# Kernel tuning notes

Measured on AMD Instinct MI355X. Metric: run time of the kernel, lower is better.

The kernel has to match this reference:

```python
import jax, jax.numpy as jnp
import numpy as np

GROUP_SIZE = 64

def _dequant(wq, scale, zero):
    # HQQ groupwise dequant: W = (Wq - zero) * scale, groups along input dim.
    out_dim, in_dim = wq.shape
    g = in_dim // GROUP_SIZE
    w = (wq.astype(jnp.float32).reshape(out_dim, g, GROUP_SIZE) - zero[:, :, None]) * scale[:, :, None]
    return w.reshape(out_dim, in_dim)

def setup_inputs() -> dict:
    key = jax.random.key(0)
    ks = jax.random.split(key, 10)
    T, H, I = 256, 4096, 14336
    G1, G2 = H // GROUP_SIZE, I // GROUP_SIZE  # 64, 224
    x = jax.random.normal(ks[0], (T, H), dtype=jnp.float32)
    w1_q = jax.random.randint(ks[1], (I, H), 0, 16, dtype=jnp.int32)
    w1_scale = jax.random.uniform(ks[2], (I, G1), dtype=jnp.float32) * 0.02
    w1_zero = jax.random.uniform(ks[3], (I, G1), dtype=jnp.float32) * 8.0
    w3_q = jax.random.randint(ks[4], (I, H), 0, 16, dtype=jnp.int32)
    w3_scale = jax.random.uniform(ks[5], (I, G1), dtype=jnp.float32) * 0.02
    w3_zero = jax.random.uniform(ks[6], (I, G1), dtype=jnp.float32) * 8.0
    w2_q = jax.random.randint(ks[7], (H, I), 0, 16, dtype=jnp.int32)
    w2_scale = jax.random.uniform(ks[8], (H, G2), dtype=jnp.float32) * 0.02
    w2_zero = jax.random.uniform(ks[9], (H, G2), dtype=jnp.float32) * 8.0
    return {"x": x, "w1_q": w1_q, "w1_scale": w1_scale, "w1_zero": w1_zero,
            "w3_q": w3_q, "w3_scale": w3_scale, "w3_zero": w3_zero,
            "w2_q": w2_q, "w2_scale": w2_scale, "w2_zero": w2_zero}

def reference(x, w1_q, w1_scale, w1_zero, w3_q, w3_scale, w3_zero, w2_q, w2_scale, w2_zero):
    w1 = _dequant(w1_q, w1_scale, w1_zero)  # [I, H]
    w3 = _dequant(w3_q, w3_scale, w3_zero)  # [I, H]
    w2 = _dequant(w2_q, w2_scale, w2_zero)  # [H, I]
    gate = jax.nn.silu(jnp.einsum('th,ih->ti', x, w1))  # [T, I]
    up = jnp.einsum('th,ih->ti', x, w3)                 # [T, I]
    return jnp.einsum('ti,hi->th', gate * up, w2)       # [T, H]
```

## Files before the change

### kernel.cpp

```cpp
#include <hip/hip_runtime.h>
#include <cstdint>
#include <cstddef>

#define T_DIM 256
#define H_DIM 4096
#define I_DIM 14336

typedef __attribute__((ext_vector_type(8))) short s8v;
typedef __attribute__((ext_vector_type(4))) short s4v;
typedef __attribute__((ext_vector_type(4))) float f4v;

static constexpr size_t XS_BYTES   = (size_t)T_DIM * H_DIM * 2;
static constexpr size_t ACT_OFF    = XS_BYTES;
static constexpr size_t ACT_BYTES  = (size_t)T_DIM * I_DIM * 2;
static constexpr size_t PART_OFF   = ACT_OFF + ACT_BYTES;
static constexpr size_t PART_BYTES = 4ull * T_DIM * H_DIM * 4;
static constexpr size_t WS_NEEDED  = PART_OFF + PART_BYTES;

__device__ __forceinline__ unsigned short f2bf(float f) {
    unsigned u = __builtin_bit_cast(unsigned, f);
    u += 0x7fffu + ((u >> 16) & 1u);
    return (unsigned short)(u >> 16);
}

__device__ __forceinline__ void bar_read() {
    __builtin_amdgcn_sched_barrier(0);
    __builtin_amdgcn_s_barrier();
    __builtin_amdgcn_sched_barrier(0);
}
__device__ __forceinline__ void bar_write() {
    __builtin_amdgcn_sched_barrier(0);
    asm volatile("s_waitcnt lgkmcnt(0)" ::: "memory");
    __builtin_amdgcn_s_barrier();
    __builtin_amdgcn_sched_barrier(0);
}

__device__ __forceinline__ s4v dq4(const int4 q, float s, float ns) {
    union { unsigned short u[4]; s4v v; } r;
    r.u[0] = f2bf(fmaf((float)q.x, s, ns));
    r.u[1] = f2bf(fmaf((float)q.y, s, ns));
    r.u[2] = f2bf(fmaf((float)q.z, s, ns));
    r.u[3] = f2bf(fmaf((float)q.w, s, ns));
    return r.v;
}

__global__ __launch_bounds__(256) void k_prep(const float* __restrict__ x,
                                              unsigned short* __restrict__ xs) {
    int i = (blockIdx.x * 256 + threadIdx.x) * 8;
    float4 a = *(const float4*)(x + i);
    float4 b = *(const float4*)(x + i + 4);
    union { unsigned short u[8]; s8v v; } r;
    r.u[0] = f2bf(a.x); r.u[1] = f2bf(a.y); r.u[2] = f2bf(a.z); r.u[3] = f2bf(a.w);
    r.u[4] = f2bf(b.x); r.u[5] = f2bf(b.y); r.u[6] = f2bf(b.z); r.u[7] = f2bf(b.w);
    *(s8v*)(xs + i) = r.v;
}

struct S1 { int4 q1, q3; float s1, z1, s3, z3; };

__global__ __launch_bounds__(512, 4) void k_gemm1(
    const int* __restrict__ w1q, const float* __restrict__ w1s, const float* __restrict__ w1z,
    const int* __restrict__ w3q, const float* __restrict__ w3s, const float* __restrict__ w3z,
    const unsigned short* __restrict__ xs, unsigned short* __restrict__ act)
{
    __shared__ unsigned char lds[2][8192];
    const int tid  = threadIdx.x;
    const int swz  = (blockIdx.x & 7) * 56 + (blockIdx.x >> 3);
    const int n0   = swz * 32;
    const int wid  = tid >> 6;
    const int lane = tid & 63;
    const int lr   = lane & 15;
    const int lkb  = lane >> 4;

    const int row = tid >> 4, h = tid & 15;
    const int4* w1p = (const int4*)w1q + (size_t)(n0 + row) * 1024;
    const int4* w3p = (const int4*)w3q + (size_t)(n0 + row) * 1024;
    const float* s1p = w1s + (size_t)(n0 + row) * 64;
    const float* z1p = w1z + (size_t)(n0 + row) * 64;
    const float* s3p = w3s + (size_t)(n0 + row) * 64;
    const float* z3p = w3z + (size_t)(n0 + row) * 64;
    const int wbyte = row * 128 + (((h >> 1) ^ (row & 7)) << 4) + ((h & 1) << 3);

    const unsigned char* xsb = (const unsigned char*)xs;

    f4v accg[2][2], accu[2][2];
    const f4v fz = {0.f, 0.f, 0.f, 0.f};
    #pragma unroll
    for (int i = 0; i < 2; ++i)
        #pragma unroll
        for (int j = 0; j < 2; ++j) { accg[i][j] = fz; accu[i][j] = fz; }

    auto load = [&](int kt, S1& p) {
        p.q1 = w1p[kt * 16 + h];
        p.q3 = w3p[kt * 16 + h];
        p.s1 = s1p[kt]; p.z1 = z1p[kt];
        p.s3 = s3p[kt]; p.z3 = z3p[kt];
    };
    auto store = [&](const S1& p, unsigned char* b) {
        *(s4v*)(b + wbyte)        = dq4(p.q1, p.s1, -p.z1 * p.s1);
        *(s4v*)(b + 4096 + wbyte) = dq4(p.q3, p.s3, -p.z3 * p.s3);
    };
    auto compute = [&](const unsigned char* b, int kt) {
        #pragma unroll
        for (int kf = 0; kf < 2; ++kf) {
            const int sw = kf * 4 + lkb;
            s8v a[2], b1[2], b3[2];
            #pragma unroll
            for (int nf = 0; nf < 2; ++nf) {
                const int rbo = (nf * 16 + lr) * 128 + ((sw ^ (lr & 7)) << 4);
                b1[nf] = *(const s8v*)(b + rbo);
                b3[nf] = *(const s8v*)(b + 4096 + rbo);
            }
            #pragma unroll
            for (int mf = 0; mf < 2; ++mf)
                a[mf] = *(const s8v*)(xsb + (size_t)(wid * 32 + mf * 16 + lr) * 8192
                                          + kt * 128 + kf * 64 + lkb * 16);
            #pragma unroll
            for (int mf = 0; mf < 2; ++mf)
                #pragma unroll
                for (int nf = 0; nf < 2; ++nf) {
                    accg[mf][nf] = __builtin_amdgcn_mfma_f32_16x16x32_bf16(a[mf], b1[nf], accg[mf][nf], 0, 0, 0);
                    accu[mf][nf] = __builtin_amdgcn_mfma_f32_16x16x32_bf16(a[mf], b3[nf], accu[mf][nf], 0, 0, 0);
                }
        }
    };

    S1 A, B;
    load(0, A);
    store(A, lds[0]);
    load(1, B);
    bar_write();

    for (int it = 0; it < 32; ++it) {
        const int t = it * 2;
        load(t + 2 > 63 ? 63 : t + 2, A);
        compute(lds[0], t);
        bar_read();
        store(B, lds[1]);
        bar_write();
        load(t + 3 > 63 ? 63 : t + 3, B);
        compute(lds[1], t + 1);
        bar_read();
        store(A, lds[0]);
        bar_write();
    }

    unsigned char* actb = (unsigned char*)act;
    #pragma unroll
    for (int mf = 0; mf < 2; ++mf)
        #pragma unroll
        for (int nf = 0; nf < 2; ++nf)
            #pragma unroll
            for (int r = 0; r < 4; ++r) {
                const int m = wid * 32 + mf * 16 + lkb * 4 + r;
                const int n = n0 + nf * 16 + lr;
                float g = accg[mf][nf][r];
                float u = accu[mf][nf][r];
                float sg = g / (1.0f + __expf(-g));
                *(unsigned short*)(actb + (size_t)m * (I_DIM * 2) + n * 2) = f2bf(sg * u);
            }
}

struct S2 { int4 q2; float s2, z2; };

template<bool ATOMIC>
__global__ __launch_bounds__(512, 4) void k_gemm2(
    const int* __restrict__ w2q, const float* __restrict__ w2s, const float* __restrict__ w2z,
    const unsigned short* __restrict__ act, float* __restrict__ outp)
{
    __shared__ unsigned char lds[2][4096];
    const int tid  = threadIdx.x;
    const int swz  = (blockIdx.x & 7) * 64 + (blockIdx.x >> 3);
    const int kc   = swz >> 7;
    const int nb   = swz & 127;
    const int n0   = nb * 32;
    const int wid  = tid >> 6;
    const int lane = tid & 63;
    const int lr   = lane & 15;
    const int lkb  = lane >> 4;

    const int row = tid >> 4, h = tid & 15;
    const int4* w2p = (const int4*)w2q + (size_t)(n0 + row) * 3584 + (size_t)kc * 896;
    const float* s2p = w2s + (size_t)(n0 + row) * 224 + kc * 56;
    const float* z2p = w2z + (size_t)(n0 + row) * 224 + kc * 56;
    const int wbyte = row * 128 + (((h >> 1) ^ (row & 7)) << 4) + ((h & 1) << 3);

    const unsigned char* actb = (const unsigned char*)act;
    const size_t akc = (size_t)kc * 7168;

    f4v acc[2][2];
    const f4v fz = {0.f, 0.f, 0.f, 0.f};
    #pragma unroll
    for (int i = 0; i < 2; ++i) { acc[i][0] = fz; acc[i][1] = fz; }

    auto load = [&](int kt, S2& p) {
        p.q2 = w2p[kt * 16 + h];
        p.s2 = s2p[kt]; p.z2 = z2p[kt];
    };
    auto store = [&](const S2& p, unsigned char* b) {
        *(s4v*)(b + wbyte) = dq4(p.q2, p.s2, -p.z2 * p.s2);
    };
    auto compute = [&](const unsigned char* b, int kt) {
        #pragma unroll
        for (int kf = 0; kf < 2; ++kf) {
            const int sw = kf * 4 + lkb;
            s8v a[2], b2[2];
            #pragma unroll
            for (int nf = 0; nf < 2; ++nf)
                b2[nf] = *(const s8v*)(b + (nf * 16 + lr) * 128 + ((sw ^ (lr & 7)) << 4));
            #pragma unroll
            for (int mf = 0; mf < 2; ++mf)
                a[mf] = *(const s8v*)(actb + (size_t)(wid * 32 + mf * 16 + lr) * (I_DIM * 2)
                                          + akc + kt * 128 + kf * 64 + lkb * 16);
            #pragma unroll
            for (int mf = 0; mf < 2; ++mf)
                #pragma unroll
                for (int nf = 0; nf < 2; ++nf)
                    acc[mf][nf] = __builtin_amdgcn_mfma_f32_16x16x32_bf16(a[mf], b2[nf], acc[mf][nf], 0, 0, 0);
        }
    };

    S2 A, B;
    load(0, A);
    store(A, lds[0]);
    load(1, B);
    bar_write();

    for (int it = 0; it < 28; ++it) {
        const int t = it * 2;
        load(t + 2 > 55 ? 55 : t + 2, A);
        compute(lds[0], t);
        bar_read();
        store(B, lds[1]);
        bar_write();
        load(t + 3 > 55 ? 55 : t + 3, B);
        compute(lds[1], t + 1);
        bar_read();
        store(A, lds[0]);
        bar_write();
    }

    float* pout = outp + (ATOMIC ? 0 : (size_t)kc * ((size_t)T_DIM * H_DIM));
    #pragma unroll
    for (int mf = 0; mf < 2; ++mf)
        #pragma unroll
        for (int nf = 0; nf < 2; ++nf)
            #pragma unroll
            for (int r = 0; r < 4; ++r) {
                const int m = wid * 32 + mf * 16 + lkb * 4 + r;
                const int n = n0 + nf * 16 + lr;
                if (ATOMIC) atomicAdd(&outp[(size_t)m * H_DIM + n], acc[mf][nf][r]);
                else        pout[(size_t)m * H_DIM + n] = acc[mf][nf][r];
            }
}

__global__ __launch_bounds__(256) void k_reduce(const f4v* __restrict__ p,
                                                f4v* __restrict__ o) {
    int i = blockIdx.x * 256 + threadIdx.x;
    f4v s = p[i];
    #pragma unroll
    for (int c = 1; c < 4; ++c) s += p[(size_t)c * 262144 + i];
    o[i] = s;
}

__global__ __launch_bounds__(256) void k_zero(f4v* __restrict__ o) {
    o[blockIdx.x * 256 + threadIdx.x] = (f4v){0.f, 0.f, 0.f, 0.f};
}

extern "C" void kernel_launch(void* const* d_in, const int* in_sizes, int n_in,
                              void* d_out, int out_size, void* d_ws, size_t ws_size,
                              hipStream_t stream) {
    const float* x   = (const float*)d_in[0];
    const int*   w1q = (const int*)  d_in[1];
    const float* w1s = (const float*)d_in[2];
    const float* w1z = (const float*)d_in[3];
    const int*   w3q = (const int*)  d_in[4];
    const float* w3s = (const float*)d_in[5];
    const float* w3z = (const float*)d_in[6];
    const int*   w2q = (const int*)  d_in[7];
    const float* w2s = (const float*)d_in[8];
    const float* w2z = (const float*)d_in[9];
    float* outp = (float*)d_out;

    unsigned short* xs  = (unsigned short*)d_ws;
    unsigned short* act = (unsigned short*)((char*)d_ws + ACT_OFF);
    float*          prt = (float*)((char*)d_ws + PART_OFF);
    const bool partials = (ws_size >= WS_NEEDED);

    k_prep<<<512, 256, 0, stream>>>(x, xs);
    k_gemm1<<<448, 512, 0, stream>>>(w1q, w1s, w1z, w3q, w3s, w3z, xs, act);
    if (partials) {
        k_gemm2<false><<<512, 512, 0, stream>>>(w2q, w2s, w2z, act, prt);
        k_reduce<<<1024, 256, 0, stream>>>((const f4v*)prt, (f4v*)outp);
    } else {
        k_zero<<<1024, 256, 0, stream>>>((f4v*)outp);
        k_gemm2<true><<<512, 512, 0, stream>>>(w2q, w2s, w2z, act, outp);
    }
}
```

Before: 334.9 us.

## Stage activations into LDS via async global_load_lds with deeper pipelining

Activations (bf16 x and the intermediate act) are re-laid out in MFMA fragment order so each block can copy whole k-tiles into a 4-deep LDS ring with direct global-to-LDS loads, instead of each wave reading A fragments straight from global memory. Weight register prefetch is deepened to four stages, with explicit vmcnt waits, and block swizzles are changed. The LDS footprint grows to roughly 140KB per block, which drops occupancy to one block per CU, and the hand-tuned vmcnt counts must match the exact number of issued loads.

```diff
diff --git a/kernel.cpp b/kernel.cpp
--- a/kernel.cpp
+++ b/kernel.cpp
@@ -21,6 +21,13 @@
     unsigned u = __builtin_bit_cast(unsigned, f);
     u += 0x7fffu + ((u >> 16) & 1u);
     return (unsigned short)(u >> 16);
+}
+
+__device__ __forceinline__ void g2lds16(const void* g, void* l) {
+    __builtin_amdgcn_global_load_lds(
+        (const __attribute__((address_space(1))) unsigned int*)g,
+        (__attribute__((address_space(3))) unsigned int*)l,
+        16, 0, 0);
 }
 
 __device__ __forceinline__ void bar_read() {
@@ -46,26 +53,31 @@
 
 __global__ __launch_bounds__(256) void k_prep(const float* __restrict__ x,
                                               unsigned short* __restrict__ xs) {
-    int i = (blockIdx.x * 256 + threadIdx.x) * 8;
-    float4 a = *(const float4*)(x + i);
-    float4 b = *(const float4*)(x + i + 4);
+    int t = blockIdx.x * 256 + threadIdx.x;
+    int l = t & 63, f = t >> 6;
+    int msub = f & 15, ksub = f >> 4;
+    int m = msub * 16 + (l & 15);
+    int k = ksub * 32 + (l >> 4) * 8;
+    const float* xp = x + (size_t)m * H_DIM + k;
+    float4 a = *(const float4*)xp;
+    float4 b = *(const float4*)(xp + 4);
     union { unsigned short u[8]; s8v v; } r;
     r.u[0] = f2bf(a.x); r.u[1] = f2bf(a.y); r.u[2] = f2bf(a.z); r.u[3] = f2bf(a.w);
     r.u[4] = f2bf(b.x); r.u[5] = f2bf(b.y); r.u[6] = f2bf(b.z); r.u[7] = f2bf(b.w);
-    *(s8v*)(xs + i) = r.v;
-}
-
-struct S1 { int4 q1, q3; float s1, z1, s3, z3; };
-
-__global__ __launch_bounds__(512, 4) void k_gemm1(
+    *((s8v*)xs + t) = r.v;
+}
+
+struct W1R { int4 q1, q3; float s1, z1, s3, z3; };
+
+__global__ __launch_bounds__(512) void k_gemm1(
     const int* __restrict__ w1q, const float* __restrict__ w1s, const float* __restrict__ w1z,
     const int* __restrict__ w3q, const float* __restrict__ w3s, const float* __restrict__ w3z,
     const unsigned short* __restrict__ xs, unsigned short* __restrict__ act)
 {
-    __shared__ unsigned char lds[2][8192];
+    __shared__ unsigned char lds[147456];
     const int tid  = threadIdx.x;
-    const int swz  = (blockIdx.x & 7) * 56 + (blockIdx.x >> 3);
-    const int n0   = swz * 32;
+    const int blk  = blockIdx.x;
+    const int n0   = blk * 32;
     const int wid  = tid >> 6;
     const int lane = tid & 63;
     const int lr   = lane & 15;
@@ -78,7 +90,7 @@
     const float* z1p = w1z + (size_t)(n0 + row) * 64;
     const float* s3p = w3s + (size_t)(n0 + row) * 64;
     const float* z3p = w3z + (size_t)(n0 + row) * 64;
-    const int wbyte = row * 128 + (((h >> 1) ^ (row & 7)) << 4) + ((h & 1) << 3);
+    const int wbyte = row * 128 + ((((h >> 1) ^ (row & 7)) << 4) | ((h & 1) << 3));
 
     const unsigned char* xsb = (const unsigned char*)xs;
 
@@ -89,31 +101,38 @@
         #pragma unroll
         for (int j = 0; j < 2; ++j) { accg[i][j] = fz; accu[i][j] = fz; }
 
-    auto load = [&](int kt, S1& p) {
+    auto xl = [&](int t) -> unsigned char* { return lds + (size_t)(t & 3) * 32768; };
+    auto wl = [&](int t) -> unsigned char* { return lds + 131072 + (size_t)(t & 1) * 8192; };
+
+    auto wload = [&](int kt, W1R& p) {
         p.q1 = w1p[kt * 16 + h];
         p.q3 = w3p[kt * 16 + h];
-        p.s1 = s1p[kt]; p.z1 = z1p[kt];
-        p.s3 = s3p[kt]; p.z3 = z3p[kt];
-    };
-    auto store = [&](const S1& p, unsigned char* b) {
+        p.s1 = s1p[kt]; p.z1 = z1p[kt]; p.s3 = s3p[kt]; p.z3 = z3p[kt];
+    };
+    auto xstage = [&](int kt, unsigned char* dst) {
+        const unsigned char* src = xsb + (size_t)kt * 32768 + (size_t)(wid * 4) * 1024
+                                       + (size_t)lane * 16;
+        #pragma unroll
+        for (int j = 0; j < 4; ++j)
+            g2lds16(src + j * 1024, dst + (wid * 4 + j) * 1024);
+    };
+    auto wstore = [&](const W1R& p, unsigned char* b) {
         *(s4v*)(b + wbyte)        = dq4(p.q1, p.s1, -p.z1 * p.s1);
         *(s4v*)(b + 4096 + wbyte) = dq4(p.q3, p.s3, -p.z3 * p.s3);
     };
-    auto compute = [&](const unsigned char* b, int kt) {
+    auto compute = [&](const unsigned char* xb, const unsigned char* wb) {
         #pragma unroll
         for (int kf = 0; kf < 2; ++kf) {
-            const int sw = kf * 4 + lkb;
             s8v a[2], b1[2], b3[2];
             #pragma unroll
+            for (int mf = 0; mf < 2; ++mf)
+                a[mf] = *(const s8v*)(xb + (kf * 16 + wid * 2 + mf) * 1024 + lane * 16);
+            #pragma unroll
             for (int nf = 0; nf < 2; ++nf) {
-                const int rbo = (nf * 16 + lr) * 128 + ((sw ^ (lr & 7)) << 4);
-                b1[nf] = *(const s8v*)(b + rbo);
-                b3[nf] = *(const s8v*)(b + 4096 + rbo);
+                const int rbo = (nf * 16 + lr) * 128 + (((kf * 4 + lkb) ^ (lr & 7)) << 4);
+                b1[nf] = *(const s8v*)(wb + rbo);
+                b3[nf] = *(const s8v*)(wb + 4096 + rbo);
             }
-            #pragma unroll
-            for (int mf = 0; mf < 2; ++mf)
-                a[mf] = *(const s8v*)(xsb + (size_t)(wid * 32 + mf * 16 + lr) * 8192
-                                          + kt * 128 + kf * 64 + lkb * 16);
             #pragma unroll
             for (int mf = 0; mf < 2; ++mf)
                 #pragma unroll
@@ -124,54 +143,66 @@
         }
     };
 
-    S1 A, B;
-    load(0, A);
-    store(A, lds[0]);
-    load(1, B);
+    W1R R0, R1, R2, R3;
+    wload(0, R0);
+    wload(1, R1); xstage(0, xl(0));
+    wload(2, R2); xstage(1, xl(1));
+    wload(3, R3); xstage(2, xl(2));
+    wstore(R0, wl(0));
     bar_write();
 
-    for (int it = 0; it < 32; ++it) {
-        const int t = it * 2;
-        load(t + 2 > 63 ? 63 : t + 2, A);
-        compute(lds[0], t);
+    auto step = [&](int t, W1R& Rld, const W1R& Rst) {
+        wload((t + 4) & 63, Rld);
+        __builtin_amdgcn_sched_barrier(0);
+        xstage((t + 3) & 63, xl(t + 3));
+        __builtin_amdgcn_sched_barrier(0);
+        asm volatile("s_waitcnt vmcnt(26)" ::: "memory");
+        __builtin_amdgcn_sched_barrier(0);
+        compute(xl(t), wl(t));
         bar_read();
-        store(B, lds[1]);
+        wstore(Rst, wl(t + 1));
         bar_write();
-        load(t + 3 > 63 ? 63 : t + 3, B);
-        compute(lds[1], t + 1);
-        bar_read();
-        store(A, lds[0]);
-        bar_write();
+    };
+    for (int i = 0; i < 16; ++i) {
+        const int t = i * 4;
+        step(t + 0, R0, R1);
+        step(t + 1, R1, R2);
+        step(t + 2, R2, R3);
+        step(t + 3, R3, R0);
     }
 
     unsigned char* actb = (unsigned char*)act;
     #pragma unroll
-    for (int mf = 0; mf < 2; ++mf)
+    for (int mf = 0; mf < 2; ++mf) {
+        const int msub = wid * 2 + mf;
         #pragma unroll
         for (int nf = 0; nf < 2; ++nf)
             #pragma unroll
             for (int r = 0; r < 4; ++r) {
-                const int m = wid * 32 + mf * 16 + lkb * 4 + r;
-                const int n = n0 + nf * 16 + lr;
+                const int mrow  = lkb * 4 + r;
+                const int n     = nf * 16 + lr;
+                const int lanef = mrow + (n >> 3) * 16;
                 float g = accg[mf][nf][r];
                 float u = accu[mf][nf][r];
                 float sg = g / (1.0f + __expf(-g));
-                *(unsigned short*)(actb + (size_t)m * (I_DIM * 2) + n * 2) = f2bf(sg * u);
+                *(unsigned short*)(actb + (size_t)(blk * 16 + msub) * 1024
+                                        + lanef * 16 + (n & 7) * 2) = f2bf(sg * u);
             }
-}
-
-struct S2 { int4 q2; float s2, z2; };
+    }
+}
+
+struct W2R { int4 q2; float s2, z2; };
 
 template<bool ATOMIC>
-__global__ __launch_bounds__(512, 4) void k_gemm2(
+__global__ __launch_bounds__(512) void k_gemm2(
     const int* __restrict__ w2q, const float* __restrict__ w2s, const float* __restrict__ w2z,
     const unsigned short* __restrict__ act, float* __restrict__ outp)
 {
-    __shared__ unsigned char lds[2][4096];
+    __shared__ unsigned char lds[139264];
     const int tid  = threadIdx.x;
-    const int swz  = (blockIdx.x & 7) * 64 + (blockIdx.x >> 3);
-    const int kc   = swz >> 7;
-    const int nb   = swz & 127;
+    const int bx   = blockIdx.x;
+    const int kc   = (bx & 7) >> 1;
+    const int nb   = (bx >> 3) * 2 + (bx & 1);
     const int n0   = nb * 32;
     const int wid  = tid >> 6;
     const int lane = tid & 63;
@@ -179,38 +210,49 @@
     const int lkb  = lane >> 4;
 
     const int row = tid >> 4, h = tid & 15;
-    const int4* w2p = (const int4*)w2q + (size_t)(n0 + row) * 3584 + (size_t)kc * 896;
-    const float* s2p = w2s + (size_t)(n0 + row) * 224 + kc * 56;
-    const float* z2p = w2z + (size_t)(n0 + row) * 224 + kc * 56;
-    const int wbyte = row * 128 + (((h >> 1) ^ (row & 7)) << 4) + ((h & 1) << 3);
+    const int4* w2p = (const int4*)w2q + (size_t)(n0 + row) * 3584;
+    const float* s2p = w2s + (size_t)(n0 + row) * 224;
+    const float* z2p = w2z + (size_t)(n0 + row) * 224;
+    const int wbyte = row * 128 + ((((h >> 1) ^ (row & 7)) << 4) | ((h & 1) << 3));
 
     const unsigned char* actb = (const unsigned char*)act;
-    const size_t akc = (size_t)kc * 7168;
+    const int kt0 = kc * 56;
 
     f4v acc[2][2];
     const f4v fz = {0.f, 0.f, 0.f, 0.f};
     #pragma unroll
     for (int i = 0; i < 2; ++i) { acc[i][0] = fz; acc[i][1] = fz; }
 
-    auto load = [&](int kt, S2& p) {
-        p.q2 = w2p[kt * 16 + h];
-        p.s2 = s2p[kt]; p.z2 = z2p[kt];
-    };
-    auto store = [&](const S2& p, unsigned char* b) {
+    auto xl = [&](int t) -> unsigned char* { return lds + (size_t)(t & 3) * 32768; };
+    auto wl = [&](int t) -> unsigned char* { return lds + 131072 + (size_t)(t & 1) * 4096; };
+    auto wrap = [](int v) { return v >= 56 ? v - 56 : v; };
+
+    auto wload = [&](int ktL, W2R& p) {
+        const int ktg = kt0 + ktL;
+        p.q2 = w2p[ktg * 16 + h];
+        p.s2 = s2p[ktg]; p.z2 = z2p[ktg];
+    };
+    auto xstage = [&](int ktL, unsigned char* dst) {
+        const unsigned char* src = actb + (size_t)(kt0 + ktL) * 32768
+                                        + (size_t)(wid * 4) * 1024 + (size_t)lane * 16;
+        #pragma unroll
+        for (int j = 0; j < 4; ++j)
+            g2lds16(src + j * 1024, dst + (wid * 4 + j) * 1024);
+    };
+    auto wstore = [&](const W2R& p, unsigned char* b) {
         *(s4v*)(b + wbyte) = dq4(p.q2, p.s2, -p.z2 * p.s2);
     };
-    auto compute = [&](const unsigned char* b, int kt) {
+    auto compute = [&](const unsigned char* xb, const unsigned char* wb) {
         #pragma unroll
         for (int kf = 0; kf < 2; ++kf) {
-            const int sw = kf * 4 + lkb;
             s8v a[2], b2[2];
             #pragma unroll
+            for (int mf = 0; mf < 2; ++mf)
+                a[mf] = *(const s8v*)(xb + (kf * 16 + wid * 2 + mf) * 1024 + lane * 16);
+            #pragma unroll
             for (int nf = 0; nf < 2; ++nf)
-                b2[nf] = *(const s8v*)(b + (nf * 16 + lr) * 128 + ((sw ^ (lr & 7)) << 4));
-            #pragma unroll
-            for (int mf = 0; mf < 2; ++mf)
-                a[mf] = *(const s8v*)(actb + (size_t)(wid * 32 + mf * 16 + lr) * (I_DIM * 2)
-                                          + akc + kt * 128 + kf * 64 + lkb * 16);
+                b2[nf] = *(const s8v*)(wb + (nf * 16 + lr) * 128
+                                          + (((kf * 4 + lkb) ^ (lr & 7)) << 4));
             #pragma unroll
             for (int mf = 0; mf < 2; ++mf)
                 #pragma unroll
@@ -219,24 +261,32 @@
         }
     };
 
-    S2 A, B;
-    load(0, A);
-    store(A, lds[0]);
-    load(1, B);
+    W2R R0, R1, R2, R3;
+    wload(0, R0);
+    wload(1, R1); xstage(0, xl(0));
+    wload(2, R2); xstage(1, xl(1));
+    wload(3, R3); xstage(2, xl(2));
+    wstore(R0, wl(0));
     bar_write();
 
-    for (int it = 0; it < 28; ++it) {
-        const int t = it * 2;
-        load(t + 2 > 55 ? 55 : t + 2, A);
-        compute(lds[0], t);
+    auto step = [&](int t, W2R& Rld, const W2R& Rst) {
+        wload(wrap(t + 4), Rld);
+        __builtin_amdgcn_sched_barrier(0);
+        xstage(wrap(t + 3), xl(t + 3));
+        __builtin_amdgcn_sched_barrier(0);
+        asm volatile("s_waitcnt vmcnt(17)" ::: "memory");
+        __builtin_amdgcn_sched_barrier(0);
+        compute(xl(t), wl(t));
         bar_read();
-        store(B, lds[1]);
+        wstore(Rst, wl(t + 1));
         bar_write();
-        load(t + 3 > 55 ? 55 : t + 3, B);
-        compute(lds[1], t + 1);
-        bar_read();
-        store(A, lds[0]);
-        bar_write();
+    };
+    for (int i = 0; i < 14; ++i) {
+        const int t = i * 4;
+        step(t + 0, R0, R1);
+        step(t + 1, R1, R2);
+        step(t + 2, R2, R3);
+        step(t + 3, R3, R0);
     }
 
     float* pout = outp + (ATOMIC ? 0 : (size_t)kc * ((size_t)T_DIM * H_DIM));
```

Result: faster. 297.8 us (-11.1%).

## Pre-tile activations into MFMA fragment layout and stage them via global_load_lds

Applied to the files above, without the earlier changes.

Writes the bf16 input and the intermediate activation in a fragment-ordered tiled layout so each wave reads contiguous 1KB chunks. Both GEMMs now stage their activation tiles into LDS with direct global-to-LDS loads, double-buffered alongside the dequantized weights, instead of loading activation fragments straight from global memory. GEMM1 is re-split into 256-thread blocks that cover half the token rows and 32 columns (896 blocks), and the wave-level weight mapping is changed to match. This trades extra LDS use and an extra barrier per step for coalesced, reused activation loads.

```diff
diff --git a/kernel.cpp b/kernel.cpp
--- a/kernel.cpp
+++ b/kernel.cpp
@@ -10,12 +10,12 @@
 typedef __attribute__((ext_vector_type(4))) short s4v;
 typedef __attribute__((ext_vector_type(4))) float f4v;
 
-static constexpr size_t XS_BYTES   = (size_t)T_DIM * H_DIM * 2;
-static constexpr size_t ACT_OFF    = XS_BYTES;
-static constexpr size_t ACT_BYTES  = (size_t)T_DIM * I_DIM * 2;
-static constexpr size_t PART_OFF   = ACT_OFF + ACT_BYTES;
-static constexpr size_t PART_BYTES = 4ull * T_DIM * H_DIM * 4;
-static constexpr size_t WS_NEEDED  = PART_OFF + PART_BYTES;
+static constexpr size_t XS_OFF    = 0;
+static constexpr size_t ACT_OFF   = (size_t)T_DIM * H_DIM * 2;
+static constexpr size_t ACT_BYTES = (size_t)T_DIM * I_DIM * 2;
+static constexpr size_t PRT_OFF   = ACT_OFF + ACT_BYTES;
+static constexpr size_t PRT_BYTES = 4ull * T_DIM * H_DIM * 4;
+static constexpr size_t WS_NEED   = PRT_OFF + PRT_BYTES;
 
 __device__ __forceinline__ unsigned short f2bf(float f) {
     unsigned u = __builtin_bit_cast(unsigned, f);
@@ -23,16 +23,11 @@
     return (unsigned short)(u >> 16);
 }
 
-__device__ __forceinline__ void bar_read() {
-    __builtin_amdgcn_sched_barrier(0);
-    __builtin_amdgcn_s_barrier();
-    __builtin_amdgcn_sched_barrier(0);
-}
-__device__ __forceinline__ void bar_write() {
-    __builtin_amdgcn_sched_barrier(0);
-    asm volatile("s_waitcnt lgkmcnt(0)" ::: "memory");
-    __builtin_amdgcn_s_barrier();
-    __builtin_amdgcn_sched_barrier(0);
+__device__ __forceinline__ void g2lds16(const void* g, void* l) {
+    __builtin_amdgcn_global_load_lds(
+        (const __attribute__((address_space(1))) unsigned int*)g,
+        (__attribute__((address_space(3))) unsigned int*)l,
+        16, 0, 0);
 }
 
 __device__ __forceinline__ s4v dq4(const int4 q, float s, float ns) {
@@ -46,197 +41,207 @@
 
 __global__ __launch_bounds__(256) void k_prep(const float* __restrict__ x,
                                               unsigned short* __restrict__ xs) {
-    int i = (blockIdx.x * 256 + threadIdx.x) * 8;
-    float4 a = *(const float4*)(x + i);
-    float4 b = *(const float4*)(x + i + 4);
+    int t = blockIdx.x * 256 + threadIdx.x;
+    int m = t >> 9, slot = t & 511;
+    int k0 = slot * 8;
+    const float* xp = x + (size_t)m * H_DIM + k0;
+    float4 a = *(const float4*)xp;
+    float4 b = *(const float4*)(xp + 4);
     union { unsigned short u[8]; s8v v; } r;
     r.u[0] = f2bf(a.x); r.u[1] = f2bf(a.y); r.u[2] = f2bf(a.z); r.u[3] = f2bf(a.w);
     r.u[4] = f2bf(b.x); r.u[5] = f2bf(b.y); r.u[6] = f2bf(b.z); r.u[7] = f2bf(b.w);
-    *(s8v*)(xs + i) = r.v;
-}
-
-struct S1 { int4 q1, q3; float s1, z1, s3, z3; };
-
-__global__ __launch_bounds__(512, 4) void k_gemm1(
+    int idx16 = ((k0 >> 6) * 2 + (m >> 7)) * 16 + ((k0 >> 5) & 1) * 8 + ((m >> 4) & 7);
+    int lane  = (m & 15) + 16 * ((k0 >> 3) & 3);
+    *(s8v*)((unsigned char*)xs + (size_t)idx16 * 1024 + lane * 16) = r.v;
+}
+
+struct W1R { int4 q1a, q1b, q3a, q3b;
+             float s1a, z1a, s1b, z1b, s3a, z3a, s3b, z3b; };
+
+__global__ __launch_bounds__(256, 3) void k_gemm1(
     const int* __restrict__ w1q, const float* __restrict__ w1s, const float* __restrict__ w1z,
     const int* __restrict__ w3q, const float* __restrict__ w3s, const float* __restrict__ w3z,
-    const unsigned short* __restrict__ xs, unsigned short* __restrict__ act)
+    const unsigned char* __restrict__ xs, unsigned char* __restrict__ act)
 {
-    __shared__ unsigned char lds[2][8192];
-    const int tid  = threadIdx.x;
-    const int swz  = (blockIdx.x & 7) * 56 + (blockIdx.x >> 3);
-    const int n0   = swz * 32;
-    const int wid  = tid >> 6;
-    const int lane = tid & 63;
-    const int lr   = lane & 15;
-    const int lkb  = lane >> 4;
+    __shared__ unsigned char xbuf[2][16384];
+    __shared__ unsigned char wbuf[2][8192];
+    const int tid = threadIdx.x;
+    const int bx  = blockIdx.x;
+    const int nb  = (bx >> 4) * 8 + (bx & 7);
+    const int mh  = (bx >> 3) & 1;
+    const int n0  = nb * 32;
+    const int wid = tid >> 6, l = tid & 63;
+    const int lr  = l & 15, lk = l >> 4;
 
     const int row = tid >> 4, h = tid & 15;
-    const int4* w1p = (const int4*)w1q + (size_t)(n0 + row) * 1024;
-    const int4* w3p = (const int4*)w3q + (size_t)(n0 + row) * 1024;
-    const float* s1p = w1s + (size_t)(n0 + row) * 64;
-    const float* z1p = w1z + (size_t)(n0 + row) * 64;
-    const float* s3p = w3s + (size_t)(n0 + row) * 64;
-    const float* z3p = w3z + (size_t)(n0 + row) * 64;
-    const int wbyte = row * 128 + (((h >> 1) ^ (row & 7)) << 4) + ((h & 1) << 3);
-
-    const unsigned char* xsb = (const unsigned char*)xs;
-
-    f4v accg[2][2], accu[2][2];
+    const int4* w1lo = (const int4*)w1q + (size_t)(n0 + row) * 1024;
+    const int4* w1hi = w1lo + (size_t)16 * 1024;
+    const int4* w3lo = (const int4*)w3q + (size_t)(n0 + row) * 1024;
+    const int4* w3hi = w3lo + (size_t)16 * 1024;
+    const float* s1lo = w1s + (size_t)(n0 + row) * 64; const float* s1hi = s1lo + 16 * 64;
+    const float* z1lo = w1z + (size_t)(n0 + row) * 64; const float* z1hi = z1lo + 16 * 64;
+    const float* s3lo = w3s + (size_t)(n0 + row) * 64; const float* s3hi = s3lo + 16 * 64;
+    const float* z3lo = w3z + (size_t)(n0 + row) * 64; const float* z3hi = z3lo + 16 * 64;
+    const int wlane = row + 16 * ((h & 7) >> 1);
+    const int ks_s  = h >> 3;
+    const int wb0 = (ks_s * 2 + 0) * 1024 + wlane * 16 + (h & 1) * 8;
+    const int wb1 = (ks_s * 2 + 1) * 1024 + wlane * 16 + (h & 1) * 8;
+
+    f4v ag[2][2], au[2][2];
     const f4v fz = {0.f, 0.f, 0.f, 0.f};
     #pragma unroll
     for (int i = 0; i < 2; ++i)
         #pragma unroll
-        for (int j = 0; j < 2; ++j) { accg[i][j] = fz; accu[i][j] = fz; }
-
-    auto load = [&](int kt, S1& p) {
-        p.q1 = w1p[kt * 16 + h];
-        p.q3 = w3p[kt * 16 + h];
-        p.s1 = s1p[kt]; p.z1 = z1p[kt];
-        p.s3 = s3p[kt]; p.z3 = z3p[kt];
-    };
-    auto store = [&](const S1& p, unsigned char* b) {
-        *(s4v*)(b + wbyte)        = dq4(p.q1, p.s1, -p.z1 * p.s1);
-        *(s4v*)(b + 4096 + wbyte) = dq4(p.q3, p.s3, -p.z3 * p.s3);
-    };
-    auto compute = [&](const unsigned char* b, int kt) {
-        #pragma unroll
-        for (int kf = 0; kf < 2; ++kf) {
-            const int sw = kf * 4 + lkb;
-            s8v a[2], b1[2], b3[2];
-            #pragma unroll
-            for (int nf = 0; nf < 2; ++nf) {
-                const int rbo = (nf * 16 + lr) * 128 + ((sw ^ (lr & 7)) << 4);
-                b1[nf] = *(const s8v*)(b + rbo);
-                b3[nf] = *(const s8v*)(b + 4096 + rbo);
-            }
-            #pragma unroll
-            for (int mf = 0; mf < 2; ++mf)
-                a[mf] = *(const s8v*)(xsb + (size_t)(wid * 32 + mf * 16 + lr) * 8192
-                                          + kt * 128 + kf * 64 + lkb * 16);
-            #pragma unroll
-            for (int mf = 0; mf < 2; ++mf)
-                #pragma unroll
-                for (int nf = 0; nf < 2; ++nf) {
-                    accg[mf][nf] = __builtin_amdgcn_mfma_f32_16x16x32_bf16(a[mf], b1[nf], accg[mf][nf], 0, 0, 0);
-                    accu[mf][nf] = __builtin_amdgcn_mfma_f32_16x16x32_bf16(a[mf], b3[nf], accu[mf][nf], 0, 0, 0);
-                }
+        for (int j = 0; j < 2; ++j) { ag[i][j] = fz; au[i][j] = fz; }
+
+    auto wload = [&](int kt, W1R& w) {
+        w.q1a = w1lo[kt * 16 + h]; w.q1b = w1hi[kt * 16 + h];
+        w.q3a = w3lo[kt * 16 + h]; w.q3b = w3hi[kt * 16 + h];
+        w.s1a = s1lo[kt]; w.z1a = z1lo[kt]; w.s1b = s1hi[kt]; w.z1b = z1hi[kt];
+        w.s3a = s3lo[kt]; w.z3a = z3lo[kt]; w.s3b = s3hi[kt]; w.z3b = z3hi[kt];
+    };
+    auto wstore = [&](const W1R& w, unsigned char* b) {
+        *(s4v*)(b + wb0)        = dq4(w.q1a, w.s1a, -w.z1a * w.s1a);
+        *(s4v*)(b + wb1)        = dq4(w.q1b, w.s1b, -w.z1b * w.s1b);
+        *(s4v*)(b + 4096 + wb0) = dq4(w.q3a, w.s3a, -w.z3a * w.s3a);
+        *(s4v*)(b + 4096 + wb1) = dq4(w.q3b, w.s3b, -w.z3b * w.s3b);
+    };
+    auto xstage = [&](int kt, unsigned char* dst) {
+        const unsigned char* src = xs + (size_t)(kt * 2 + mh) * 16384
+                                      + wid * 4096 + (size_t)l * 16;
+        unsigned char* d = dst + wid * 4096;
+        #pragma unroll
+        for (int j = 0; j < 4; ++j)
+            g2lds16(src + j * 1024, d + j * 1024);
+    };
+    auto compute = [&](const unsigned char* xb, const unsigned char* wb) {
+        #pragma unroll
+        for (int ks = 0; ks < 2; ++ks) {
+            s8v a0  = *(const s8v*)(xb + (ks * 8 + wid * 2 + 0) * 1024 + l * 16);
+            s8v a1  = *(const s8v*)(xb + (ks * 8 + wid * 2 + 1) * 1024 + l * 16);
+            s8v b1a = *(const s8v*)(wb + (ks * 2 + 0) * 1024 + l * 16);
+            s8v b1b = *(const s8v*)(wb + (ks * 2 + 1) * 1024 + l * 16);
+            s8v b3a = *(const s8v*)(wb + 4096 + (ks * 2 + 0) * 1024 + l * 16);
+            s8v b3b = *(const s8v*)(wb + 4096 + (ks * 2 + 1) * 1024 + l * 16);
+            ag[0][0] = __builtin_amdgcn_mfma_f32_16x16x32_bf16(a0, b1a, ag[0][0], 0, 0, 0);
+            ag[1][0] = __builtin_amdgcn_mfma_f32_16x16x32_bf16(a1, b1a, ag[1][0], 0, 0, 0);
+            ag[0][1] = __builtin_amdgcn_mfma_f32_16x16x32_bf16(a0, b1b, ag[0][1], 0, 0, 0);
+            ag[1][1] = __builtin_amdgcn_mfma_f32_16x16x32_bf16(a1, b1b, ag[1][1], 0, 0, 0);
+            au[0][0] = __builtin_amdgcn_mfma_f32_16x16x32_bf16(a0, b3a, au[0][0], 0, 0, 0);
+            au[1][0] = __builtin_amdgcn_mfma_f32_16x16x32_bf16(a1, b3a, au[1][0], 0, 0, 0);
+            au[0][1] = __builtin_amdgcn_mfma_f32_16x16x32_bf16(a0, b3b, au[0][1], 0, 0, 0);
+            au[1][1] = __builtin_amdgcn_mfma_f32_16x16x32_bf16(a1, b3b, au[1][1], 0, 0, 0);
         }
     };
 
-    S1 A, B;
-    load(0, A);
-    store(A, lds[0]);
-    load(1, B);
-    bar_write();
-
-    for (int it = 0; it < 32; ++it) {
-        const int t = it * 2;
-        load(t + 2 > 63 ? 63 : t + 2, A);
-        compute(lds[0], t);
-        bar_read();
-        store(B, lds[1]);
-        bar_write();
-        load(t + 3 > 63 ? 63 : t + 3, B);
-        compute(lds[1], t + 1);
-        bar_read();
-        store(A, lds[0]);
-        bar_write();
+    W1R W;
+    wload(0, W);
+    xstage(0, xbuf[0]);
+    wstore(W, wbuf[0]);
+    __syncthreads();
+
+    for (int t = 0; t < 64; ++t) {
+        const int cur = t & 1;
+        if (t < 63) {
+            wload(t + 1, W);
+            xstage(t + 1, xbuf[cur ^ 1]);
+        }
+        __builtin_amdgcn_sched_barrier(0);
+        compute(xbuf[cur], wbuf[cur]);
+        __syncthreads();
+        if (t < 63) wstore(W, wbuf[cur ^ 1]);
+        __syncthreads();
     }
 
-    unsigned char* actb = (unsigned char*)act;
     #pragma unroll
     for (int mf = 0; mf < 2; ++mf)
         #pragma unroll
         for (int nf = 0; nf < 2; ++nf)
             #pragma unroll
             for (int r = 0; r < 4; ++r) {
-                const int m = wid * 32 + mf * 16 + lkb * 4 + r;
-                const int n = n0 + nf * 16 + lr;
-                float g = accg[mf][nf][r];
-                float u = accu[mf][nf][r];
+                float g = ag[mf][nf][r], u = au[mf][nf][r];
                 float sg = g / (1.0f + __expf(-g));
-                *(unsigned short*)(actb + (size_t)m * (I_DIM * 2) + n * 2) = f2bf(sg * u);
+                const int idx16 = (nb >> 1) * 32 + (nb & 1) * 16 + mh * 8 + wid * 2 + mf;
+                const int lane2 = (lk * 4 + r) + 16 * (nf * 2 + (lr >> 3));
+                *(unsigned short*)(act + (size_t)idx16 * 1024 + lane2 * 16
+                                       + (lr & 7) * 2) = f2bf(sg * u);
             }
 }
 
-struct S2 { int4 q2; float s2, z2; };
+struct W2R { int4 q2; float s2, z2; };
 
 template<bool ATOMIC>
 __global__ __launch_bounds__(512, 4) void k_gemm2(
     const int* __restrict__ w2q, const float* __restrict__ w2s, const float* __restrict__ w2z,
-    const unsigned short* __restrict__ act, float* __restrict__ outp)
+    const unsigned char* __restrict__ act, float* __restrict__ outp)
 {
-    __shared__ unsigned char lds[2][4096];
-    const int tid  = threadIdx.x;
-    const int swz  = (blockIdx.x & 7) * 64 + (blockIdx.x >> 3);
-    const int kc   = swz >> 7;
-    const int nb   = swz & 127;
-    const int n0   = nb * 32;
-    const int wid  = tid >> 6;
-    const int lane = tid & 63;
-    const int lr   = lane & 15;
-    const int lkb  = lane >> 4;
+    __shared__ unsigned char xbuf[2][32768];
+    __shared__ unsigned char wbuf[2][4096];
+    const int tid = threadIdx.x;
+    const int bx  = blockIdx.x;
+    const int kc  = (bx & 7) >> 1;
+    const int nb  = (bx >> 3) * 2 + (bx & 1);
+    const int n0  = nb * 32;
+    const int wid = tid >> 6, l = tid & 63;
+    const int lr  = l & 15, lk = l >> 4;
 
     const int row = tid >> 4, h = tid & 15;
     const int4* w2p = (const int4*)w2q + (size_t)(n0 + row) * 3584 + (size_t)kc * 896;
     const float* s2p = w2s + (size_t)(n0 + row) * 224 + kc * 56;
     const float* z2p = w2z + (size_t)(n0 + row) * 224 + kc * 56;
-    const int wbyte = row * 128 + (((h >> 1) ^ (row & 7)) << 4) + ((h & 1) << 3);
-
-    const unsigned char* actb = (const unsigned char*)act;
-    const size_t akc = (size_t)kc * 7168;
+    const int wlane = (row & 15) + 16 * ((h & 7) >> 1);
+    const int wb    = ((h >> 3) * 2 + (row >> 4)) * 1024 + wlane * 16 + (h & 1) * 8;
 
     f4v acc[2][2];
     const f4v fz = {0.f, 0.f, 0.f, 0.f};
-    #pragma unroll
-    for (int i = 0; i < 2; ++i) { acc[i][0] = fz; acc[i][1] = fz; }
-
-    auto load = [&](int kt, S2& p) {
-        p.q2 = w2p[kt * 16 + h];
-        p.s2 = s2p[kt]; p.z2 = z2p[kt];
-    };
-    auto store = [&](const S2& p, unsigned char* b) {
-        *(s4v*)(b + wbyte) = dq4(p.q2, p.s2, -p.z2 * p.s2);
-    };
-    auto compute = [&](const unsigned char* b, int kt) {
-        #pragma unroll
-        for (int kf = 0; kf < 2; ++kf) {
-            const int sw = kf * 4 + lkb;
-            s8v a[2], b2[2];
-            #pragma unroll
-            for (int nf = 0; nf < 2; ++nf)
-                b2[nf] = *(const s8v*)(b + (nf * 16 + lr) * 128 + ((sw ^ (lr & 7)) << 4));
-            #pragma unroll
-            for (int mf = 0; mf < 2; ++mf)
-                a[mf] = *(const s8v*)(actb + (size_t)(wid * 32 + mf * 16 + lr) * (I_DIM * 2)
-                                          + akc + kt * 128 + kf * 64 + lkb * 16);
-            #pragma unroll
-            for (int mf = 0; mf < 2; ++mf)
-                #pragma unroll
-                for (int nf = 0; nf < 2; ++nf)
-                    acc[mf][nf] = __builtin_amdgcn_mfma_f32_16x16x32_bf16(a[mf], b2[nf], acc[mf][nf], 0, 0, 0);
+    acc[0][0] = fz; acc[0][1] = fz; acc[1][0] = fz; acc[1][1] = fz;
+
+    auto wload = [&](int kt, W2R& w) {
+        w.q2 = w2p[kt * 16 + h];
+        w.s2 = s2p[kt]; w.z2 = z2p[kt];
+    };
+    auto wstore = [&](const W2R& w, unsigned char* b) {
+        *(s4v*)(b + wb) = dq4(w.q2, w.s2, -w.z2 * w.s2);
+    };
+    auto xstage = [&](int kt, unsigned char* dst) {
+        const unsigned char* src = act + (size_t)(kc * 56 + kt) * 32768
+                                       + wid * 4096 + (size_t)l * 16;
+        unsigned char* d = dst + wid * 4096;
+        #pragma unroll
+        for (int j = 0; j < 4; ++j)
+            g2lds16(src + j * 1024, d + j * 1024);
+    };
+    auto compute = [&](const unsigned char* xb, const unsigned char* wbp) {
+        #pragma unroll
+        for (int ks = 0; ks < 2; ++ks) {
+            s8v a0 = *(const s8v*)(xb + (ks * 16 + wid * 2 + 0) * 1024 + l * 16);
+            s8v a1 = *(const s8v*)(xb + (ks * 16 + wid * 2 + 1) * 1024 + l * 16);
+            s8v b0 = *(const s8v*)(wbp + (ks * 2 + 0) * 1024 + l * 16);
+            s8v b1 = *(const s8v*)(wbp + (ks * 2 + 1) * 1024 + l * 16);
+            acc[0][0] = __builtin_amdgcn_mfma_f32_16x16x32_bf16(a0, b0, acc[0][0], 0, 0, 0);
+            acc[1][0] = __builtin_amdgcn_mfma_f32_16x16x32_bf16(a1, b0, acc[1][0], 0, 0, 0);
+            acc[0][1] = __builtin_amdgcn_mfma_f32_16x16x32_bf16(a0, b1, acc[0][1], 0, 0, 0);
+            acc[1][1] = __builtin_amdgcn_mfma_f32_16x16x32_bf16(a1, b1, acc[1][1], 0, 0, 0);
         }
     };
 
-    S2 A, B;
-    load(0, A);
-    store(A, lds[0]);
-    load(1, B);
-    bar_write();
-
-    for (int it = 0; it < 28; ++it) {
-        const int t = it * 2;
-        load(t + 2 > 55 ? 55 : t + 2, A);
-        compute(lds[0], t);
-        bar_read();
-        store(B, lds[1]);
-        bar_write();
-        load(t + 3 > 55 ? 55 : t + 3, B);
-        compute(lds[1], t + 1);
-        bar_read();
-        store(A, lds[0]);
-        bar_write();
+    W2R W;
+    wload(0, W);
+    xstage(0, xbuf[0]);
+    wstore(W, wbuf[0]);
+    __syncthreads();
+
+    for (int t = 0; t < 56; ++t) {
+        const int cur = t & 1;
+        if (t < 55) {
+            wload(t + 1, W);
+            xstage(t + 1, xbuf[cur ^ 1]);
+        }
+        __builtin_amdgcn_sched_barrier(0);
+        compute(xbuf[cur], wbuf[cur]);
+        __syncthreads();
+        if (t < 55) wstore(W, wbuf[cur ^ 1]);
+        __syncthreads();
     }
 
     float* pout = outp + (ATOMIC ? 0 : (size_t)kc * ((size_t)T_DIM * H_DIM));
@@ -246,10 +251,10 @@
         for (int nf = 0; nf < 2; ++nf)
             #pragma unroll
             for (int r = 0; r < 4; ++r) {
-                const int m = wid * 32 + mf * 16 + lkb * 4 + r;
-                const int n = n0 + nf * 16 + lr;
-                if (ATOMIC) atomicAdd(&outp[(size_t)m * H_DIM + n], acc[mf][nf][r]);
-                else        pout[(size_t)m * H_DIM + n] = acc[mf][nf][r];
+                const int M = wid * 32 + mf * 16 + lk * 4 + r;
+                const int N = n0 + nf * 16 + lr;
+                if (ATOMIC) atomicAdd(&outp[(size_t)M * H_DIM + N], acc[mf][nf][r]);
+                else        pout[(size_t)M * H_DIM + N] = acc[mf][nf][r];
             }
 }
 
@@ -281,13 +286,14 @@
     const float* w2z = (const float*)d_in[9];
     float* outp = (float*)d_out;
 
-    unsigned short* xs  = (unsigned short*)d_ws;
-    unsigned short* act = (unsigned short*)((char*)d_ws + ACT_OFF);
-    float*          prt = (float*)((char*)d_ws + PART_OFF);
-    const bool partials = (ws_size >= WS_NEEDED);
+    unsigned short* xs  = (unsigned short*)((char*)d_ws + XS_OFF);
+    unsigned char*  act = (unsigned char*)d_ws + ACT_OFF;
+    float*          prt = (float*)((char*)d_ws + PRT_OFF);
+    const bool partials = (ws_size >= WS_NEED);
 
     k_prep<<<512, 256, 0, stream>>>(x, xs);
-    k_gemm1<<<448, 512, 0, stream>>>(w1q, w1s, w1z, w3q, w3s, w3z, xs, act);
+    k_gemm1<<<896, 256, 0, stream>>>(w1q, w1s, w1z, w3q, w3s, w3z,
+                                     (const unsigned char*)xs, act);
     if (partials) {
         k_gemm2<false><<<512, 512, 0, stream>>>(w2q, w2s, w2z, act, prt);
         k_reduce<<<1024, 256, 0, stream>>>((const f4v*)prt, (f4v*)outp);
```

New measurement: 411.6 us. 1.23x slower.
